# Kernel tuning notes

Hardware: AMD Instinct MI355X
Metric: run time of the kernel (lower is better)

Reference implementation:

```python
import jax, jax.numpy as jnp
import numpy as np

N_NODES = 100000
N_EDGES = 1600000
D = 128          # h_size == feature_representation_size
N_CLASSES = 2
N_GRAPHS = 64


def setup_inputs() -> dict:
    key = jax.random.key(0)
    ks = jax.random.split(key, 8)
    scale = 1.0 / np.sqrt(D)
    x = jax.random.normal(ks[0], (N_NODES, D), jnp.float32)
    edge_index = jax.random.randint(ks[1], (2, N_EDGES), 0, N_NODES, dtype=jnp.int64)
    batch = jnp.sort(jax.random.randint(ks[2], (N_NODES,), 0, N_GRAPHS, dtype=jnp.int64))
    W0 = jax.random.normal(ks[3], (D, D), jnp.float32) * scale
    W1 = jax.random.normal(ks[4], (D, D), jnp.float32) * scale
    W2 = jax.random.normal(ks[5], (D, D), jnp.float32) * scale
    Wf = jax.random.normal(ks[6], (D, N_CLASSES), jnp.float32) * scale
    return dict(
        x=x, edge_index=edge_index, batch=batch,
        W0=W0, b0=jnp.zeros((D,), jnp.float32),
        W1=W1, b1=jnp.zeros((D,), jnp.float32),
        W2=W2, b2=jnp.zeros((D,), jnp.float32),
        Wf=Wf, bf=jnp.zeros((N_CLASSES,), jnp.float32),
    )


def gcn_norm(edge_index, num_nodes):
    # add self loops, symmetric normalization D^{-1/2} A_hat D^{-1/2}
    src, dst = edge_index[0], edge_index[1]
    loop = jnp.arange(num_nodes, dtype=src.dtype)
    src = jnp.concatenate([src, loop])
    dst = jnp.concatenate([dst, loop])
    ew = jnp.ones(src.shape[0], jnp.float32)
    deg = jax.ops.segment_sum(ew, dst, num_segments=num_nodes)
    dinv = jnp.where(deg > 0, jax.lax.rsqrt(deg), 0.0)
    norm = dinv[src] * dinv[dst]  # [E+N]
    return src, dst, norm


def gcn_conv(h, W, b, src, dst, norm, num_nodes):
    h = h @ W                                   # linear transform
    msg = h[src] * norm[:, None]                # gather + scale over edges
    out = jax.ops.segment_sum(msg, dst, num_segments=num_nodes)  # scatter-add
    return out + b


def reference(x, edge_index, batch, W0, b0, W1, b1, W2, b2, Wf, bf):
    n = x.shape[0]
    src, dst, norm = gcn_norm(edge_index, n)
    h = jax.nn.relu(gcn_conv(x, W0, b0, src, dst, norm, n))
    h = jax.nn.relu(gcn_conv(h, W1, b1, src, dst, norm, n))
    h = gcn_conv(h, W2, b2, src, dst, norm, n)  # last layer, no relu
    pooled = jax.ops.segment_max(h, batch, num_segments=N_GRAPHS)  # global max pool
    return pooled @ Wf + bf
```

## Files before the change

kernel.cpp:

```cpp
#include <hip/hip_runtime.h>
#include <hip/hip_bf16.h>
#include <hip/hip_fp16.h>
#include <float.h>

#define D 128
#define NGRAPHS 64
#define BKSHIFT 9
#define BKNODES 512
#define MAXBK 256
#define PCH 4096

typedef _Float16 h8 __attribute__((ext_vector_type(8)));
typedef float f4 __attribute__((ext_vector_type(4)));

__device__ __forceinline__ unsigned fkey(float f){
  unsigned u = __float_as_uint(f);
  return (u & 0x80000000u) ? ~u : (u | 0x80000000u);
}
__device__ __forceinline__ float funkey(unsigned k){
  unsigned u = (k & 0x80000000u) ? (k ^ 0x80000000u) : ~k;
  return __uint_as_float(u);
}

__global__ __launch_bounds__(256) void k_bhist_w(const int* __restrict__ dst,
    int* __restrict__ bcnt, int E, int npart,
    const float* __restrict__ W0, const float* __restrict__ W1,
    const float* __restrict__ W2, _Float16* __restrict__ Wsw){
  if ((int)blockIdx.x >= npart){
    int layer = blockIdx.x - npart;
    const float* W = (layer == 0) ? W0 : (layer == 1) ? W1 : W2;
    _Float16* dstp = Wsw + (size_t)layer * 16384;
    int lane = threadIdx.x & 63;
    int quad = lane >> 4;
    int n    = lane & 15;
    for (int pair = (threadIdx.x >> 6); pair < 32; pair += 4){
      int k0 = pair >> 3;
      int tt = pair & 7;
      _Float16 v[8];
      #pragma unroll
      for (int j = 0; j < 8; j++){
        int k = k0 * 32 + quad * 8 + j;
        v[j] = (_Float16)W[k * 128 + 16 * tt + n];
      }
      *(uint4*)&dstp[((size_t)pair * 64 + lane) * 8] = *(uint4*)v;
    }
    return;
  }
  __shared__ int h[MAXBK];
  int t = threadIdx.x;
  for (int i = t; i < MAXBK; i += 256) h[i] = 0;
  __syncthreads();
  int e0 = blockIdx.x * PCH;
  #pragma unroll
  for (int j = 0; j < PCH / 256; j++){
    int e = e0 + t + j * 256;
    if (e < E) atomicAdd(&h[dst[e] >> BKSHIFT], 1);
  }
  __syncthreads();
  for (int i = t; i < MAXBK; i += 256) if (h[i]) atomicAdd(&bcnt[i], h[i]);
}

__global__ __launch_bounds__(256) void k_bscan(const int* __restrict__ bcnt,
    int* __restrict__ bOff, int* __restrict__ bCur, int* __restrict__ row_ptr,
    unsigned* __restrict__ pk, int nbk, int N, int E){
  __shared__ int sh[256];
  int t = threadIdx.x;
  for (int i = t; i < NGRAPHS * D; i += 256) pk[i] = 0u;
  int v = (t < nbk) ? bcnt[t] : 0;
  sh[t] = v; __syncthreads();
  for (int off = 1; off < 256; off <<= 1){
    int x = (t >= off) ? sh[t - off] : 0;
    __syncthreads();
    sh[t] += x;
    __syncthreads();
  }
  if (t < nbk){ int ex = sh[t] - v; bOff[t] = ex; bCur[t] = ex; }
  if (t == 0){ bOff[nbk] = E; row_ptr[N] = E; }
}

__global__ __launch_bounds__(256) void k_part(const int* __restrict__ src,
    const int* __restrict__ dst, int* __restrict__ bCur,
    uint2* __restrict__ epart, int E){
  __shared__ int scnt[MAXBK], soff[MAXBK], sbase[MAXBK], scur[MAXBK];
  __shared__ int stmp[256];
  __shared__ uint2 stage[PCH];
  int t = threadIdx.x;
  int e0 = blockIdx.x * PCH;
  int eN = E - e0; if (eN > PCH) eN = PCH;
  for (int i = t; i < MAXBK; i += 256){ scnt[i] = 0; scur[i] = 0; }
  __syncthreads();
  uint2 mye[PCH / 256];
  #pragma unroll
  for (int j = 0; j < PCH / 256; j++){
    int e = e0 + t + j * 256;
    if (e < E){
      mye[j].x = (unsigned)src[e];
      mye[j].y = (unsigned)dst[e];
      atomicAdd(&scnt[mye[j].y >> BKSHIFT], 1);
    }
  }
  __syncthreads();
  int v = scnt[t];
  stmp[t] = v; __syncthreads();
  for (int off = 1; off < 256; off <<= 1){
    int x = (t >= off) ? stmp[t - off] : 0;
    __syncthreads();
    stmp[t] += x;
    __syncthreads();
  }
  soff[t] = stmp[t] - v;
  if (v > 0) sbase[t] = atomicAdd(&bCur[t], v);
  __syncthreads();
  #pragma unroll
  for (int j = 0; j < PCH / 256; j++){
    int e = e0 + t + j * 256;
    if (e < E){
      int b = mye[j].y >> BKSHIFT;
      int l = atomicAdd(&scur[b], 1);
      stage[soff[b] + l] = mye[j];
    }
  }
  __syncthreads();
  for (int j = t; j < eN; j += 256){
    uint2 ed = stage[j];
    int b = (int)(ed.y >> BKSHIFT);
    epart[(size_t)sbase[b] + (j - soff[b])] = ed;
  }
}

__global__ __launch_bounds__(256) void k_bfill(const uint2* __restrict__ epart,
    const int* __restrict__ bOff, int* __restrict__ row_ptr,
    int* __restrict__ col, float* __restrict__ dinv, int N){
  __shared__ int hc[BKNODES], off[BKNODES], cur[BKNODES];
  __shared__ int stmp[256];
  int b = blockIdx.x, t = threadIdx.x;
  int base = bOff[b], cntE = bOff[b + 1] - base;
  int node0 = b << BKSHIFT;
  int nloc = N - node0; if (nloc > BKNODES) nloc = BKNODES;
  for (int i = t; i < BKNODES; i += 256) hc[i] = 0;
  __syncthreads();
  for (int j = t; j < cntE; j += 256){
    uint2 ed = epart[(size_t)base + j];
    atomicAdd(&hc[ed.y - node0], 1);
  }
  __syncthreads();
  int a0 = hc[2 * t], a1 = hc[2 * t + 1];
  int s = a0 + a1;
  stmp[t] = s; __syncthreads();
  for (int o = 1; o < 256; o <<= 1){
    int x = (t >= o) ? stmp[t - o] : 0;
    __syncthreads();
    stmp[t] += x;
    __syncthreads();
  }
  int ex = stmp[t] - s;
  off[2 * t] = ex; off[2 * t + 1] = ex + a0;
  __syncthreads();
  for (int i = t; i < nloc; i += 256){
    row_ptr[node0 + i] = base + off[i];
    dinv[node0 + i]    = rsqrtf((float)hc[i] + 1.0f);
    cur[i] = off[i];
  }
  __syncthreads();
  for (int j = t; j < cntE; j += 256){
    uint2 ed = epart[(size_t)base + j];
    int p = atomicAdd(&cur[ed.y - node0], 1);
    col[base + p] = (int)ed.x;
  }
}

__global__ __launch_bounds__(256) void gemm_mfma(const _Float16* __restrict__ A,
    const _Float16* __restrict__ Wsw, _Float16* __restrict__ C, int M){
  __shared__ _Float16 lds[4][16][136];
  int wave = threadIdx.x >> 6;
  int lane = threadIdx.x & 63;
  int quad = lane >> 4;
  int l15  = lane & 15;
  int m0 = blockIdx.x * 64 + wave * 16;
  if (m0 >= M) return;
  f4 acc[8] = {};
  h8 af[4];
  const _Float16* arow = A + (size_t)(m0 + l15) * D;
  #pragma unroll
  for (int k0 = 0; k0 < 4; k0++)
    af[k0] = *(const h8*)&arow[k0 * 32 + quad * 8];
  #pragma unroll
  for (int k0 = 0; k0 < 4; k0++){
    #pragma unroll
    for (int t = 0; t < 8; t++){
      h8 bf = *(const h8*)&Wsw[((size_t)(k0 * 8 + t) * 64 + lane) * 8];
      acc[t] = __builtin_amdgcn_mfma_f32_16x16x32_f16(af[k0], bf, acc[t], 0, 0, 0);
    }
  }
  #pragma unroll
  for (int t = 0; t < 8; t++){
    #pragma unroll
    for (int r = 0; r < 4; r++)
      lds[wave][quad * 4 + r][t * 16 + l15] = (_Float16)acc[t][r];
  }
  #pragma unroll
  for (int it = 0; it < 4; it++){
    int idx = it * 64 + lane;
    int row = idx >> 4;
    int ch  = idx & 15;
    *(uint4*)&C[(size_t)(m0 + row) * D + ch * 8] = *(uint4*)&lds[wave][row][ch * 8];
  }
}

__global__ __launch_bounds__(256) void gemm_mfma_f32A(const float* __restrict__ A,
    const _Float16* __restrict__ Wsw, _Float16* __restrict__ C, int M){
  __shared__ _Float16 lds[4][16][136];
  int wave = threadIdx.x >> 6;
  int lane = threadIdx.x & 63;
  int quad = lane >> 4;
  int l15  = lane & 15;
  int m0 = blockIdx.x * 64 + wave * 16;
  if (m0 >= M) return;
  f4 acc[8] = {};
  h8 af[4];
  const float* arow = A + (size_t)(m0 + l15) * D;
  #pragma unroll
  for (int k0 = 0; k0 < 4; k0++){
    float4 a = *(const float4*)&arow[k0 * 32 + quad * 8];
    float4 b = *(const float4*)&arow[k0 * 32 + quad * 8 + 4];
    __half2 p0 = __floats2half2_rn(a.x, a.y);
    __half2 p1 = __floats2half2_rn(a.z, a.w);
    __half2 p2 = __floats2half2_rn(b.x, b.y);
    __half2 p3 = __floats2half2_rn(b.z, b.w);
    union { uint4 u; h8 v; } cv;
    cv.u.x = *(unsigned*)&p0; cv.u.y = *(unsigned*)&p1;
    cv.u.z = *(unsigned*)&p2; cv.u.w = *(unsigned*)&p3;
    af[k0] = cv.v;
  }
  #pragma unroll
  for (int k0 = 0; k0 < 4; k0++){
    #pragma unroll
    for (int t = 0; t < 8; t++){
      h8 bf = *(const h8*)&Wsw[((size_t)(k0 * 8 + t) * 64 + lane) * 8];
      acc[t] = __builtin_amdgcn_mfma_f32_16x16x32_f16(af[k0], bf, acc[t], 0, 0, 0);
    }
  }
  #pragma unroll
  for (int t = 0; t < 8; t++){
    #pragma unroll
    for (int r = 0; r < 4; r++)
      lds[wave][quad * 4 + r][t * 16 + l15] = (_Float16)acc[t][r];
  }
  #pragma unroll
  for (int it = 0; it < 4; it++){
    int idx = it * 64 + lane;
    int row = idx >> 4;
    int ch  = idx & 15;
    *(uint4*)&C[(size_t)(m0 + row) * D + ch * 8] = *(uint4*)&lds[wave][row][ch * 8];
  }
}

__device__ __forceinline__ void accm(float* acc, uint4 u, float w){
  union { uint4 u; _Float16 h[8]; } cv;
  cv.u = u;
  #pragma unroll
  for (int k = 0; k < 8; k++)
    acc[k] += (float)cv.h[k] * w;
}

__global__ __launch_bounds__(256) void k_agg(const __half* __restrict__ t,
    const int* __restrict__ row_ptr, const int* __restrict__ col,
    const float* __restrict__ dinv, const float* __restrict__ bias,
    __half* __restrict__ outh, int relu, int N){
  int node = blockIdx.x * 4 + (threadIdx.x >> 6);
  if (node >= N) return;
  int lane = threadIdx.x & 63;
  int way  = lane >> 4;
  int cg   = (lane & 15) * 8;
  float di = dinv[node];
  int beg = row_ptr[node], end = row_ptr[node + 1];
  float acc[8] = {0.f,0.f,0.f,0.f,0.f,0.f,0.f,0.f};
  int j = beg + way;
  for (; j + 12 < end; j += 16){
    int s0 = col[j], s1 = col[j + 4], s2 = col[j + 8], s3 = col[j + 12];
    float w0 = dinv[s0] * di;
    float w1 = dinv[s1] * di;
    float w2 = dinv[s2] * di;
    float w3 = dinv[s3] * di;
    uint4 u0 = *(const uint4*)&t[(size_t)s0 * D + cg];
    uint4 u1 = *(const uint4*)&t[(size_t)s1 * D + cg];
    uint4 u2 = *(const uint4*)&t[(size_t)s2 * D + cg];
    uint4 u3 = *(const uint4*)&t[(size_t)s3 * D + cg];
    accm(acc, u0, w0);
    accm(acc, u1, w1);
    accm(acc, u2, w2);
    accm(acc, u3, w3);
  }
  for (; j < end; j += 4){
    int s = col[j];
    float w = dinv[s] * di;
    uint4 u = *(const uint4*)&t[(size_t)s * D + cg];
    accm(acc, u, w);
  }
  #pragma unroll
  for (int k = 0; k < 8; k++){
    acc[k] += __shfl_xor(acc[k], 16, 64);
    acc[k] += __shfl_xor(acc[k], 32, 64);
  }
  if (way == 0){
    uint4 su = *(const uint4*)&t[(size_t)node * D + cg];
    union { uint4 u; _Float16 h[8]; } sv; sv.u = su;
    float dii = di * di;
    float4 b0 = *(const float4*)&bias[cg];
    float4 b1 = *(const float4*)&bias[cg + 4];
    float bb[8] = {b0.x, b0.y, b0.z, b0.w, b1.x, b1.y, b1.z, b1.w};
    float o[8];
    #pragma unroll
    for (int k = 0; k < 8; k++)
      o[k] = acc[k] + (float)sv.h[k] * dii + bb[k];
    if (relu){
      #pragma unroll
      for (int k = 0; k < 8; k++) o[k] = fmaxf(o[k], 0.f);
    }
    __half2 p0 = __floats2half2_rn(o[0], o[1]);
    __half2 p1 = __floats2half2_rn(o[2], o[3]);
    __half2 p2 = __floats2half2_rn(o[4], o[5]);
    __half2 p3 = __floats2half2_rn(o[6], o[7]);
    uint4 u;
    u.x = *(unsigned*)&p0; u.y = *(unsigned*)&p1;
    u.z = *(unsigned*)&p2; u.w = *(unsigned*)&p3;
    *(uint4*)&outh[(size_t)node * D + cg] = u;
  }
}

__global__ __launch_bounds__(128) void k_pool(const __half* __restrict__ h,
    const int* __restrict__ batch, unsigned* __restrict__ pk, int N){
  int d = threadIdx.x;
  int n0 = blockIdx.x * 64;
  int nEnd = n0 + 64; if (nEnd > N) nEnd = N;
  float cur = -FLT_MAX;
  int curg = batch[n0];
  int n = n0;
  for (; n + 3 < nEnd; n += 4){
    const __half* r = &h[(size_t)n * D + d];
    __half v0 = r[0], v1 = r[D], v2 = r[2 * D], v3 = r[3 * D];
    int g0 = batch[n], g1 = batch[n + 1], g2 = batch[n + 2], g3 = batch[n + 3];
    if (g0 != curg){ atomicMax(&pk[curg * D + d], fkey(cur)); cur = -FLT_MAX; curg = g0; }
    cur = fmaxf(cur, __half2float(v0));
    if (g1 != curg){ atomicMax(&pk[curg * D + d], fkey(cur)); cur = -FLT_MAX; curg = g1; }
    cur = fmaxf(cur, __half2float(v1));
    if (g2 != curg){ atomicMax(&pk[curg * D + d], fkey(cur)); cur = -FLT_MAX; curg = g2; }
    cur = fmaxf(cur, __half2float(v2));
    if (g3 != curg){ atomicMax(&pk[curg * D + d], fkey(cur)); cur = -FLT_MAX; curg = g3; }
    cur = fmaxf(cur, __half2float(v3));
  }
  for (; n < nEnd; n++){
    int g = batch[n];
    if (g != curg){ atomicMax(&pk[curg * D + d], fkey(cur)); cur = -FLT_MAX; curg = g; }
    cur = fmaxf(cur, __half2float(h[(size_t)n * D + d]));
  }
  atomicMax(&pk[curg * D + d], fkey(cur));
}

__global__ __launch_bounds__(128) void k_final(const unsigned* __restrict__ pk,
    const float* __restrict__ Wf, const float* __restrict__ bf,
    float* __restrict__ out){
  int t = threadIdx.x;
  int g = t >> 1, c = t & 1;
  float s = bf[c];
  for (int k = 0; k < D; k++)
    s += funkey(pk[g * D + k]) * Wf[k * 2 + c];
  out[g * 2 + c] = s;
}

extern "C" void kernel_launch(void* const* d_in, const int* in_sizes, int n_in,
                              void* d_out, int out_size, void* d_ws, size_t ws_size,
                              hipStream_t stream){
  const float* x   = (const float*)d_in[0];
  const int*   ei  = (const int*)d_in[1];
  const int*   bat = (const int*)d_in[2];
  const float* W0  = (const float*)d_in[3];
  const float* b0  = (const float*)d_in[4];
  const float* W1  = (const float*)d_in[5];
  const float* b1  = (const float*)d_in[6];
  const float* W2  = (const float*)d_in[7];
  const float* b2  = (const float*)d_in[8];
  const float* Wf  = (const float*)d_in[9];
  const float* bf  = (const float*)d_in[10];
  int N = in_sizes[0] / D;
  int E = in_sizes[1] / 2;
  const int* srcp = ei;
  const int* dstp = ei + E;
  int nbk   = (N + BKNODES - 1) / BKNODES;
  int npart = (E + PCH - 1) / PCH;

  char* p = (char*)d_ws;
  auto alloc = [&](size_t bytes)->char*{
    char* r = p; p += (bytes + 255) & ~(size_t)255; return r;
  };
  float*     dinv    = (float*)alloc((size_t)N * 4);
  int*       row_ptr = (int*)alloc((size_t)(N + 1) * 4);
  int*       col     = (int*)alloc((size_t)E * 4);
  uint2*     epart   = (uint2*)alloc((size_t)E * 8);
  _Float16*  tmp     = (_Float16*)alloc((size_t)N * D * 2);
  _Float16*  h16     = (_Float16*)alloc((size_t)N * D * 2);
  _Float16*  Wsw     = (_Float16*)alloc((size_t)3 * 16384 * 2);
  unsigned*  pk      = (unsigned*)alloc((size_t)NGRAPHS * D * 4);
  int*       bcnt    = (int*)alloc((size_t)MAXBK * 4);
  int*       bOff    = (int*)alloc((size_t)(MAXBK + 1) * 4);
  int*       bCur    = (int*)alloc((size_t)MAXBK * 4);

  hipMemsetAsync(bcnt, 0, (size_t)MAXBK * 4, stream);

  k_bhist_w<<<npart + 3, 256, 0, stream>>>(dstp, bcnt, E, npart, W0, W1, W2, Wsw);
  k_bscan<<<1, 256, 0, stream>>>(bcnt, bOff, bCur, row_ptr, pk, nbk, N, E);
  k_part<<<npart, 256, 0, stream>>>(srcp, dstp, bCur, epart, E);
  k_bfill<<<nbk, 256, 0, stream>>>(epart, bOff, row_ptr, col, dinv, N);

  int gblocks = (N + 63) / 64;
  int ablocks = (N + 3) / 4;
  gemm_mfma_f32A<<<gblocks, 256, 0, stream>>>(x, Wsw, tmp, N);
  k_agg<<<ablocks, 256, 0, stream>>>((const __half*)tmp, row_ptr, col, dinv, b0, (__half*)h16, 1, N);
  gemm_mfma<<<gblocks, 256, 0, stream>>>(h16, Wsw + 16384, tmp, N);
  k_agg<<<ablocks, 256, 0, stream>>>((const __half*)tmp, row_ptr, col, dinv, b1, (__half*)h16, 1, N);
  gemm_mfma<<<gblocks, 256, 0, stream>>>(h16, Wsw + 32768, tmp, N);
  k_agg<<<ablocks, 256, 0, stream>>>((const __half*)tmp, row_ptr, col, dinv, b2, (__half*)h16, 0, N);
  k_pool<<<(N + 63) / 64, 128, 0, stream>>>((const __half*)h16, bat, pk, N);
  k_final<<<1, 128, 0, stream>>>(pk, Wf, bf, (float*)d_out);
}
```

Baseline: 412.5 us.

## Fuse aggregation with next-layer GEMM and merge first GEMM into histogram launch

Adds a kernel that aggregates 16 nodes per block, applies bias and ReLU, stages the rows in LDS, and multiplies them by the next layer's weights with MFMA. This removes the intermediate h16 round trip and two standalone GEMM launches. It also folds the layer-0 GEMM, the edge histogram and the W1/W2 conversion into one kernel, and moves the bcnt zeroing into a small W0 conversion kernel instead of a memset. The cost is that each aggregation block now handles 4 nodes per wave serially, which may reduce memory-level parallelism in the gather. A second ping-pong buffer is allocated.

```diff
diff --git a/kernel.cpp b/kernel.cpp
--- a/kernel.cpp
+++ b/kernel.cpp
@@ -22,42 +22,106 @@
   return __uint_as_float(u);
 }
 
-__global__ __launch_bounds__(256) void k_bhist_w(const int* __restrict__ dst,
-    int* __restrict__ bcnt, int E, int npart,
-    const float* __restrict__ W0, const float* __restrict__ W1,
-    const float* __restrict__ W2, _Float16* __restrict__ Wsw){
-  if ((int)blockIdx.x >= npart){
-    int layer = blockIdx.x - npart;
-    const float* W = (layer == 0) ? W0 : (layer == 1) ? W1 : W2;
-    _Float16* dstp = Wsw + (size_t)layer * 16384;
+__device__ __forceinline__ void wcvt_pair(const float* __restrict__ W,
+    _Float16* __restrict__ dstp, int pair, int lane){
+  int quad = lane >> 4;
+  int n    = lane & 15;
+  int k0 = pair >> 3;
+  int tt = pair & 7;
+  _Float16 v[8];
+  #pragma unroll
+  for (int j = 0; j < 8; j++){
+    int k = k0 * 32 + quad * 8 + j;
+    v[j] = (_Float16)W[k * 128 + 16 * tt + n];
+  }
+  *(uint4*)&dstp[((size_t)pair * 64 + lane) * 8] = *(uint4*)v;
+}
+
+__global__ __launch_bounds__(256) void k_wcvt0(const float* __restrict__ W0,
+    _Float16* __restrict__ Wsw, int* __restrict__ bcnt){
+  if (blockIdx.x == 0 && threadIdx.x < MAXBK) bcnt[threadIdx.x] = 0;
+  int lane = threadIdx.x & 63;
+  int pair = blockIdx.x * 4 + (threadIdx.x >> 6);
+  wcvt_pair(W0, Wsw, pair, lane);
+}
+
+__global__ __launch_bounds__(256) void k_mega(
+    const float* __restrict__ x, const _Float16* __restrict__ Wsw0,
+    _Float16* __restrict__ C, int M, int gb,
+    const int* __restrict__ dst, int* __restrict__ bcnt, int E, int npart,
+    const float* __restrict__ W1, const float* __restrict__ W2,
+    _Float16* __restrict__ Wsw12){
+  __shared__ __align__(16) char smraw[4 * 16 * 136 * 2];
+  int bid = blockIdx.x;
+  if (bid < gb){
+    _Float16 (*lds)[136] = (_Float16(*)[136])(smraw + (threadIdx.x >> 6) * 16 * 136 * 2);
     int lane = threadIdx.x & 63;
     int quad = lane >> 4;
-    int n    = lane & 15;
-    for (int pair = (threadIdx.x >> 6); pair < 32; pair += 4){
-      int k0 = pair >> 3;
-      int tt = pair & 7;
-      _Float16 v[8];
+    int l15  = lane & 15;
+    int m0 = bid * 64 + (threadIdx.x >> 6) * 16;
+    if (m0 >= M) return;
+    f4 acc[8] = {};
+    h8 af[4];
+    const float* arow = x + (size_t)(m0 + l15) * D;
+    #pragma unroll
+    for (int k0 = 0; k0 < 4; k0++){
+      float4 a = *(const float4*)&arow[k0 * 32 + quad * 8];
+      float4 b = *(const float4*)&arow[k0 * 32 + quad * 8 + 4];
+      __half2 p0 = __floats2half2_rn(a.x, a.y);
+      __half2 p1 = __floats2half2_rn(a.z, a.w);
+      __half2 p2 = __floats2half2_rn(b.x, b.y);
+      __half2 p3 = __floats2half2_rn(b.z, b.w);
+      union { uint4 u; h8 v; } cv;
+      cv.u.x = *(unsigned*)&p0; cv.u.y = *(unsigned*)&p1;
+      cv.u.z = *(unsigned*)&p2; cv.u.w = *(unsigned*)&p3;
+      af[k0] = cv.v;
+    }
+    #pragma unroll
+    for (int k0 = 0; k0 < 4; k0++){
       #pragma unroll
-      for (int j = 0; j < 8; j++){
-        int k = k0 * 32 + quad * 8 + j;
-        v[j] = (_Float16)W[k * 128 + 16 * tt + n];
+      for (int t = 0; t < 8; t++){
+        h8 bf = *(const h8*)&Wsw0[((size_t)(k0 * 8 + t) * 64 + lane) * 8];
+        acc[t] = __builtin_amdgcn_mfma_f32_16x16x32_f16(af[k0], bf, acc[t], 0, 0, 0);
       }
-      *(uint4*)&dstp[((size_t)pair * 64 + lane) * 8] = *(uint4*)v;
+    }
+    #pragma unroll
+    for (int t = 0; t < 8; t++){
+      #pragma unroll
+      for (int r = 0; r < 4; r++)
+        lds[quad * 4 + r][t * 16 + l15] = (_Float16)acc[t][r];
+    }
+    #pragma unroll
+    for (int it = 0; it < 4; it++){
+      int idx = it * 64 + lane;
+      int row = idx >> 4;
+      int ch  = idx & 15;
+      *(uint4*)&C[(size_t)(m0 + row) * D + ch * 8] = *(uint4*)&lds[row][ch * 8];
     }
     return;
   }
-  __shared__ int h[MAXBK];
-  int t = threadIdx.x;
-  for (int i = t; i < MAXBK; i += 256) h[i] = 0;
-  __syncthreads();
-  int e0 = blockIdx.x * PCH;
-  #pragma unroll
-  for (int j = 0; j < PCH / 256; j++){
-    int e = e0 + t + j * 256;
-    if (e < E) atomicAdd(&h[dst[e] >> BKSHIFT], 1);
-  }
-  __syncthreads();
-  for (int i = t; i < MAXBK; i += 256) if (h[i]) atomicAdd(&bcnt[i], h[i]);
+  bid -= gb;
+  if (bid < npart){
+    int* h = (int*)smraw;
+    int t = threadIdx.x;
+    for (int i = t; i < MAXBK; i += 256) h[i] = 0;
+    __syncthreads();
+    int e0 = bid * PCH;
+    #pragma unroll
+    for (int j = 0; j < PCH / 256; j++){
+      int e = e0 + t + j * 256;
+      if (e < E) atomicAdd(&h[dst[e] >> BKSHIFT], 1);
+    }
+    __syncthreads();
+    for (int i = t; i < MAXBK; i += 256) if (h[i]) atomicAdd(&bcnt[i], h[i]);
+    return;
+  }
+  bid -= npart;
+  const float* W = (bid < 2) ? W1 : W2;
+  _Float16* dstp = Wsw12 + ((bid < 2) ? 0 : 16384);
+  int pbase = (bid & 1) * 16;
+  int lane = threadIdx.x & 63;
+  for (int pp = (threadIdx.x >> 6); pp < 16; pp += 4)
+    wcvt_pair(W, dstp, pbase + pp, lane);
 }
 
 __global__ __launch_bounds__(256) void k_bscan(const int* __restrict__ bcnt,
@@ -169,92 +233,6 @@
   }
 }
 
-__global__ __launch_bounds__(256) void gemm_mfma(const _Float16* __restrict__ A,
-    const _Float16* __restrict__ Wsw, _Float16* __restrict__ C, int M){
-  __shared__ _Float16 lds[4][16][136];
-  int wave = threadIdx.x >> 6;
-  int lane = threadIdx.x & 63;
-  int quad = lane >> 4;
-  int l15  = lane & 15;
-  int m0 = blockIdx.x * 64 + wave * 16;
-  if (m0 >= M) return;
-  f4 acc[8] = {};
-  h8 af[4];
-  const _Float16* arow = A + (size_t)(m0 + l15) * D;
-  #pragma unroll
-  for (int k0 = 0; k0 < 4; k0++)
-    af[k0] = *(const h8*)&arow[k0 * 32 + quad * 8];
-  #pragma unroll
-  for (int k0 = 0; k0 < 4; k0++){
-    #pragma unroll
-    for (int t = 0; t < 8; t++){
-      h8 bf = *(const h8*)&Wsw[((size_t)(k0 * 8 + t) * 64 + lane) * 8];
-      acc[t] = __builtin_amdgcn_mfma_f32_16x16x32_f16(af[k0], bf, acc[t], 0, 0, 0);
-    }
-  }
-  #pragma unroll
-  for (int t = 0; t < 8; t++){
-    #pragma unroll
-    for (int r = 0; r < 4; r++)
-      lds[wave][quad * 4 + r][t * 16 + l15] = (_Float16)acc[t][r];
-  }
-  #pragma unroll
-  for (int it = 0; it < 4; it++){
-    int idx = it * 64 + lane;
-    int row = idx >> 4;
-    int ch  = idx & 15;
-    *(uint4*)&C[(size_t)(m0 + row) * D + ch * 8] = *(uint4*)&lds[wave][row][ch * 8];
-  }
-}
-
-__global__ __launch_bounds__(256) void gemm_mfma_f32A(const float* __restrict__ A,
-    const _Float16* __restrict__ Wsw, _Float16* __restrict__ C, int M){
-  __shared__ _Float16 lds[4][16][136];
-  int wave = threadIdx.x >> 6;
-  int lane = threadIdx.x & 63;
-  int quad = lane >> 4;
-  int l15  = lane & 15;
-  int m0 = blockIdx.x * 64 + wave * 16;
-  if (m0 >= M) return;
-  f4 acc[8] = {};
-  h8 af[4];
-  const float* arow = A + (size_t)(m0 + l15) * D;
-  #pragma unroll
-  for (int k0 = 0; k0 < 4; k0++){
-    float4 a = *(const float4*)&arow[k0 * 32 + quad * 8];
-    float4 b = *(const float4*)&arow[k0 * 32 + quad * 8 + 4];
-    __half2 p0 = __floats2half2_rn(a.x, a.y);
-    __half2 p1 = __floats2half2_rn(a.z, a.w);
-    __half2 p2 = __floats2half2_rn(b.x, b.y);
-    __half2 p3 = __floats2half2_rn(b.z, b.w);
-    union { uint4 u; h8 v; } cv;
-    cv.u.x = *(unsigned*)&p0; cv.u.y = *(unsigned*)&p1;
-    cv.u.z = *(unsigned*)&p2; cv.u.w = *(unsigned*)&p3;
-    af[k0] = cv.v;
-  }
-  #pragma unroll
-  for (int k0 = 0; k0 < 4; k0++){
-    #pragma unroll
-    for (int t = 0; t < 8; t++){
-      h8 bf = *(const h8*)&Wsw[((size_t)(k0 * 8 + t) * 64 + lane) * 8];
-      acc[t] = __builtin_amdgcn_mfma_f32_16x16x32_f16(af[k0], bf, acc[t], 0, 0, 0);
-    }
-  }
-  #pragma unroll
-  for (int t = 0; t < 8; t++){
-    #pragma unroll
-    for (int r = 0; r < 4; r++)
-      lds[wave][quad * 4 + r][t * 16 + l15] = (_Float16)acc[t][r];
-  }
-  #pragma unroll
-  for (int it = 0; it < 4; it++){
-    int idx = it * 64 + lane;
-    int row = idx >> 4;
-    int ch  = idx & 15;
-    *(uint4*)&C[(size_t)(m0 + row) * D + ch * 8] = *(uint4*)&lds[wave][row][ch * 8];
-  }
-}
-
 __device__ __forceinline__ void accm(float* acc, uint4 u, float w){
   union { uint4 u; _Float16 h[8]; } cv;
   cv.u = u;
@@ -263,18 +241,9 @@
     acc[k] += (float)cv.h[k] * w;
 }
 
-__global__ __launch_bounds__(256) void k_agg(const __half* __restrict__ t,
-    const int* __restrict__ row_ptr, const int* __restrict__ col,
-    const float* __restrict__ dinv, const float* __restrict__ bias,
-    __half* __restrict__ outh, int relu, int N){
-  int node = blockIdx.x * 4 + (threadIdx.x >> 6);
-  if (node >= N) return;
-  int lane = threadIdx.x & 63;
-  int way  = lane >> 4;
-  int cg   = (lane & 15) * 8;
-  float di = dinv[node];
-  int beg = row_ptr[node], end = row_ptr[node + 1];
-  float acc[8] = {0.f,0.f,0.f,0.f,0.f,0.f,0.f,0.f};
+__device__ __forceinline__ void agg_node(const __half* __restrict__ t,
+    const int* __restrict__ col, const float* __restrict__ dinv,
+    float di, int beg, int end, int way, int cg, float* acc){
   int j = beg + way;
   for (; j + 12 < end; j += 16){
     int s0 = col[j], s1 = col[j + 4], s2 = col[j + 8], s3 = col[j + 12];
@@ -297,6 +266,95 @@
     uint4 u = *(const uint4*)&t[(size_t)s * D + cg];
     accm(acc, u, w);
   }
+}
+
+__global__ __launch_bounds__(256) void k_agg_gemm(const __half* __restrict__ t,
+    const int* __restrict__ row_ptr, const int* __restrict__ col,
+    const float* __restrict__ dinv, const float* __restrict__ bias,
+    const _Float16* __restrict__ Wsw, _Float16* __restrict__ C, int N){
+  __shared__ _Float16 ldsA[16][136];
+  int tid = threadIdx.x;
+  int wave = tid >> 6;
+  int lane = tid & 63;
+  int way  = lane >> 4;
+  int l15  = lane & 15;
+  int cg   = l15 * 8;
+  int m0 = blockIdx.x * 16;
+  for (int nn = 0; nn < 4; nn++){
+    int node = m0 + wave * 4 + nn;
+    float acc[8] = {0.f,0.f,0.f,0.f,0.f,0.f,0.f,0.f};
+    float di = 0.f; int beg = 0, end = 0;
+    if (node < N){
+      di = dinv[node];
+      beg = row_ptr[node]; end = row_ptr[node + 1];
+    }
+    agg_node(t, col, dinv, di, beg, end, way, cg, acc);
+    #pragma unroll
+    for (int k = 0; k < 8; k++){
+      acc[k] += __shfl_xor(acc[k], 16, 64);
+      acc[k] += __shfl_xor(acc[k], 32, 64);
+    }
+    if (way == 0){
+      float o[8] = {0,0,0,0,0,0,0,0};
+      if (node < N){
+        uint4 su = *(const uint4*)&t[(size_t)node * D + cg];
+        union { uint4 u; _Float16 h[8]; } sv; sv.u = su;
+        float dii = di * di;
+        float4 b0 = *(const float4*)&bias[cg];
+        float4 b1 = *(const float4*)&bias[cg + 4];
+        float bb[8] = {b0.x, b0.y, b0.z, b0.w, b1.x, b1.y, b1.z, b1.w};
+        #pragma unroll
+        for (int k = 0; k < 8; k++)
+          o[k] = fmaxf(acc[k] + (float)sv.h[k] * dii + bb[k], 0.f);
+      }
+      __half2 p0 = __floats2half2_rn(o[0], o[1]);
+      __half2 p1 = __floats2half2_rn(o[2], o[3]);
+      __half2 p2 = __floats2half2_rn(o[4], o[5]);
+      __half2 p3 = __floats2half2_rn(o[6], o[7]);
+      uint4 u;
+      u.x = *(unsigned*)&p0; u.y = *(unsigned*)&p1;
+      u.z = *(unsigned*)&p2; u.w = *(unsigned*)&p3;
+      *(uint4*)&ldsA[wave * 4 + nn][cg] = u;
+    }
+  }
+  __syncthreads();
+  h8 af[4];
+  #pragma unroll
+  for (int k0 = 0; k0 < 4; k0++)
+    af[k0] = *(const h8*)&ldsA[l15][k0 * 32 + way * 8];
+  __syncthreads();
+  f4 a0 = {}, a1 = {};
+  #pragma unroll
+  for (int k0 = 0; k0 < 4; k0++){
+    h8 bf0 = *(const h8*)&Wsw[((size_t)(k0 * 8 + wave * 2    ) * 64 + lane) * 8];
+    h8 bf1 = *(const h8*)&Wsw[((size_t)(k0 * 8 + wave * 2 + 1) * 64 + lane) * 8];
+    a0 = __builtin_amdgcn_mfma_f32_16x16x32_f16(af[k0], bf0, a0, 0, 0, 0);
+    a1 = __builtin_amdgcn_mfma_f32_16x16x32_f16(af[k0], bf1, a1, 0, 0, 0);
+  }
+  #pragma unroll
+  for (int r = 0; r < 4; r++){
+    ldsA[way * 4 + r][(wave * 2    ) * 16 + l15] = (_Float16)a0[r];
+    ldsA[way * 4 + r][(wave * 2 + 1) * 16 + l15] = (_Float16)a1[r];
+  }
+  __syncthreads();
+  int row = tid >> 4, ch = tid & 15;
+  if (m0 + row < N)
+    *(uint4*)&C[(size_t)(m0 + row) * D + ch * 8] = *(uint4*)&ldsA[row][ch * 8];
+}
+
+__global__ __launch_bounds__(256) void k_agg(const __half* __restrict__ t,
+    const int* __restrict__ row_ptr, const int* __restrict__ col,
+    const float* __restrict__ dinv, const float* __restrict__ bias,
+    __half* __restrict__ outh, int N){
+  int node = blockIdx.x * 4 + (threadIdx.x >> 6);
+  if (node >= N) return;
+  int lane = threadIdx.x & 63;
+  int way  = lane >> 4;
+  int cg   = (lane & 15) * 8;
+  float di = dinv[node];
+  int beg = row_ptr[node], end = row_ptr[node + 1];
+  float acc[8] = {0.f,0.f,0.f,0.f,0.f,0.f,0.f,0.f};
+  agg_node(t, col, dinv, di, beg, end, way, cg, acc);
   #pragma unroll
   for (int k = 0; k < 8; k++){
     acc[k] += __shfl_xor(acc[k], 16, 64);
@@ -313,10 +371,6 @@
     #pragma unroll
     for (int k = 0; k < 8; k++)
       o[k] = acc[k] + (float)sv.h[k] * dii + bb[k];
-    if (relu){
-      #pragma unroll
-      for (int k = 0; k < 8; k++) o[k] = fmaxf(o[k], 0.f);
-    }
     __half2 p0 = __floats2half2_rn(o[0], o[1]);
     __half2 p1 = __floats2half2_rn(o[2], o[3]);
     __half2 p2 = __floats2half2_rn(o[4], o[5]);
@@ -388,6 +442,7 @@
   const int* dstp = ei + E;
   int nbk   = (N + BKNODES - 1) / BKNODES;
   int npart = (E + PCH - 1) / PCH;
+  int gb    = (N + 63) / 64;
 
   char* p = (char*)d_ws;
   auto alloc = [&](size_t bytes)->char*{
@@ -398,6 +453,7 @@
   int*       col     = (int*)alloc((size_t)E * 4);
   uint2*     epart   = (uint2*)alloc((size_t)E * 8);
   _Float16*  tmp     = (_Float16*)alloc((size_t)N * D * 2);
+  _Float16*  tmp2    = (_Float16*)alloc((size_t)N * D * 2);
   _Float16*  h16     = (_Float16*)alloc((size_t)N * D * 2);
   _Float16*  Wsw     = (_Float16*)alloc((size_t)3 * 16384 * 2);
   unsigned*  pk      = (unsigned*)alloc((size_t)NGRAPHS * D * 4);
@@ -405,21 +461,20 @@
   int*       bOff    = (int*)alloc((size_t)(MAXBK + 1) * 4);
   int*       bCur    = (int*)alloc((size_t)MAXBK * 4);
 
-  hipMemsetAsync(bcnt, 0, (size_t)MAXBK * 4, stream);
-
-  k_bhist_w<<<npart + 3, 256, 0, stream>>>(dstp, bcnt, E, npart, W0, W1, W2, Wsw);
+  k_wcvt0<<<8, 256, 0, stream>>>(W0, Wsw, bcnt);
+  k_mega<<<gb + npart + 4, 256, 0, stream>>>(x, Wsw, tmp, N, gb,
+      dstp, bcnt, E, npart, W1, W2, Wsw + 16384);
   k_bscan<<<1, 256, 0, stream>>>(bcnt, bOff, bCur, row_ptr, pk, nbk, N, E);
   k_part<<<npart, 256, 0, stream>>>(srcp, dstp, bCur, epart, E);
   k_bfill<<<nbk, 256, 0, stream>>>(epart, bOff, row_ptr, col, dinv, N);
 
-  int gblocks = (N + 63) / 64;
-  int ablocks = (N + 3) / 4;
-  gemm_mfma_f32A<<<gblocks, 256, 0, stream>>>(x, Wsw, tmp, N);
-  k_agg<<<ablocks, 256, 0, stream>>>((const __half*)tmp, row_ptr, col, dinv, b0, (__half*)h16, 1, N);
-  gemm_mfma<<<gblocks, 256, 0, stream>>>(h16, Wsw + 16384, tmp, N);
-  k_agg<<<ablocks, 256, 0, stream>>>((const __half*)tmp, row_ptr, col, dinv, b1, (__half*)h16, 1, N);
-  gemm_mfma<<<gblocks, 256, 0, stream>>>(h16, Wsw + 32768, tmp, N);
-  k_agg<<<ablocks, 256, 0, stream>>>((const __half*)tmp, row_ptr, col, dinv, b2, (__half*)h16, 0, N);
+  int fblocks = (N + 15) / 16;
+  k_agg_gemm<<<fblocks, 256, 0, stream>>>((const __half*)tmp, row_ptr, col,
+      dinv, b0, Wsw + 16384, tmp2, N);
+  k_agg_gemm<<<fblocks, 256, 0, stream>>>((const __half*)tmp2, row_ptr, col,
+      dinv, b1, Wsw + 32768, tmp, N);
+  k_agg<<<(N + 3) / 4, 256, 0, stream>>>((const __half*)tmp, row_ptr, col,
+      dinv, b2, (__half*)h16, N);
   k_pool<<<(N + 63) / 64, 128, 0, stream>>>((const __half*)h16, bat, pk, N);
   k_final<<<1, 128, 0, stream>>>(pk, Wf, bf, (float*)d_out);
 }
```

Result: no change. 409.0 us (-0.8%).

## Store features in channel-sliced layout and restructure aggregation for cache locality

Applied to the files above, without the earlier changes.

Node features are stored as eight 16-channel slices, each a contiguous N×16 array. The aggregation kernel now processes one slice per block, so the gathered working set per slice (N×32 bytes) can stay in L2/LLC across random neighbor reads. The first-layer GEMM is merged with the histogram and weight-conversion work into one launch, and the bcnt memset moves into a small W0-conversion kernel. The risks are more passes over the CSR structure (col, dinv and row_ptr are read eight times) and smaller 8-byte gathers.

```diff
diff --git a/kernel.cpp b/kernel.cpp
--- a/kernel.cpp
+++ b/kernel.cpp
@@ -13,6 +13,7 @@
 typedef _Float16 h8 __attribute__((ext_vector_type(8)));
 typedef float f4 __attribute__((ext_vector_type(4)));
 
+
 __device__ __forceinline__ unsigned fkey(float f){
   unsigned u = __float_as_uint(f);
   return (u & 0x80000000u) ? ~u : (u | 0x80000000u);
@@ -22,42 +23,113 @@
   return __uint_as_float(u);
 }
 
-__global__ __launch_bounds__(256) void k_bhist_w(const int* __restrict__ dst,
-    int* __restrict__ bcnt, int E, int npart,
-    const float* __restrict__ W0, const float* __restrict__ W1,
-    const float* __restrict__ W2, _Float16* __restrict__ Wsw){
-  if ((int)blockIdx.x >= npart){
-    int layer = blockIdx.x - npart;
-    const float* W = (layer == 0) ? W0 : (layer == 1) ? W1 : W2;
-    _Float16* dstp = Wsw + (size_t)layer * 16384;
+__device__ __forceinline__ void wcvt_pair(const float* __restrict__ W,
+    _Float16* __restrict__ dstp, int pair, int lane){
+  int quad = lane >> 4;
+  int n    = lane & 15;
+  int k0 = pair >> 3;
+  int tt = pair & 7;
+  _Float16 v[8];
+  #pragma unroll
+  for (int j = 0; j < 8; j++){
+    int k = k0 * 32 + quad * 8 + j;
+    v[j] = (_Float16)W[k * 128 + 16 * tt + n];
+  }
+  *(uint4*)&dstp[((size_t)pair * 64 + lane) * 8] = *(uint4*)v;
+}
+
+__global__ __launch_bounds__(256) void k_wcvt0(const float* __restrict__ W0,
+    _Float16* __restrict__ Wsw, int* __restrict__ bcnt){
+  if (blockIdx.x == 0 && threadIdx.x < MAXBK) bcnt[threadIdx.x] = 0;
+  int lane = threadIdx.x & 63;
+  int pair = blockIdx.x * 4 + (threadIdx.x >> 6);
+  wcvt_pair(W0, Wsw, pair, lane);
+}
+
+__device__ __forceinline__ void store_sliced(_Float16 (*lds)[136],
+    _Float16* __restrict__ CS, size_t sstr, int m0, int lane){
+  #pragma unroll
+  for (int it = 0; it < 4; it++){
+    int u = it * 64 + lane;
+    int slice = u & 7;
+    int half  = (u >> 3) & 1;
+    int row   = u >> 4;
+    *(uint4*)&CS[(size_t)slice * sstr + (size_t)(m0 + row) * 16 + half * 8] =
+        *(uint4*)&lds[row][slice * 16 + half * 8];
+  }
+}
+
+__global__ __launch_bounds__(256) void k_mega(
+    const float* __restrict__ x, const _Float16* __restrict__ Wsw0,
+    _Float16* __restrict__ CS, int M, int gb,
+    const int* __restrict__ dst, int* __restrict__ bcnt, int E, int npart,
+    const float* __restrict__ W1, const float* __restrict__ W2,
+    _Float16* __restrict__ Wsw12){
+  __shared__ __align__(16) char smraw[4 * 16 * 136 * 2];
+  int bid = blockIdx.x;
+  if (bid < gb){
+    _Float16 (*lds)[136] = (_Float16(*)[136])(smraw + (threadIdx.x >> 6) * 16 * 136 * 2);
     int lane = threadIdx.x & 63;
     int quad = lane >> 4;
-    int n    = lane & 15;
-    for (int pair = (threadIdx.x >> 6); pair < 32; pair += 4){
-      int k0 = pair >> 3;
-      int tt = pair & 7;
-      _Float16 v[8];
+    int l15  = lane & 15;
+    int m0 = bid * 64 + (threadIdx.x >> 6) * 16;
+    if (m0 >= M) return;
+    f4 acc[8] = {};
+    h8 af[4];
+    const float* arow = x + (size_t)(m0 + l15) * D;
+    #pragma unroll
+    for (int k0 = 0; k0 < 4; k0++){
+      float4 a = *(const float4*)&arow[k0 * 32 + quad * 8];
+      float4 b = *(const float4*)&arow[k0 * 32 + quad * 8 + 4];
+      __half2 p0 = __floats2half2_rn(a.x, a.y);
+      __half2 p1 = __floats2half2_rn(a.z, a.w);
+      __half2 p2 = __floats2half2_rn(b.x, b.y);
+      __half2 p3 = __floats2half2_rn(b.z, b.w);
+      union { uint4 u; h8 v; } cv;
+      cv.u.x = *(unsigned*)&p0; cv.u.y = *(unsigned*)&p1;
+      cv.u.z = *(unsigned*)&p2; cv.u.w = *(unsigned*)&p3;
+      af[k0] = cv.v;
+    }
+    #pragma unroll
+    for (int k0 = 0; k0 < 4; k0++){
       #pragma unroll
-      for (int j = 0; j < 8; j++){
-        int k = k0 * 32 + quad * 8 + j;
-        v[j] = (_Float16)W[k * 128 + 16 * tt + n];
+      for (int t = 0; t < 8; t++){
+        h8 bf = *(const h8*)&Wsw0[((size_t)(k0 * 8 + t) * 64 + lane) * 8];
+        acc[t] = __builtin_amdgcn_mfma_f32_16x16x32_f16(af[k0], bf, acc[t], 0, 0, 0);
       }
-      *(uint4*)&dstp[((size_t)pair * 64 + lane) * 8] = *(uint4*)v;
-    }
+    }
+    #pragma unroll
+    for (int t = 0; t < 8; t++){
+      #pragma unroll
+      for (int r = 0; r < 4; r++)
+        lds[quad * 4 + r][t * 16 + l15] = (_Float16)acc[t][r];
+    }
+    store_sliced(lds, CS, (size_t)M * 16, m0, lane);
     return;
   }
-  __shared__ int h[MAXBK];
-  int t = threadIdx.x;
-  for (int i = t; i < MAXBK; i += 256) h[i] = 0;
-  __syncthreads();
-  int e0 = blockIdx.x * PCH;
-  #pragma unroll
-  for (int j = 0; j < PCH / 256; j++){
-    int e = e0 + t + j * 256;
-    if (e < E) atomicAdd(&h[dst[e] >> BKSHIFT], 1);
-  }
-  __syncthreads();
-  for (int i = t; i < MAXBK; i += 256) if (h[i]) atomicAdd(&bcnt[i], h[i]);
+  bid -= gb;
+  if (bid < npart){
+    int* h = (int*)smraw;
+    int t = threadIdx.x;
+    for (int i = t; i < MAXBK; i += 256) h[i] = 0;
+    __syncthreads();
+    int e0 = bid * PCH;
+    #pragma unroll
+    for (int j = 0; j < PCH / 256; j++){
+      int e = e0 + t + j * 256;
+      if (e < E) atomicAdd(&h[dst[e] >> BKSHIFT], 1);
+    }
+    __syncthreads();
+    for (int i = t; i < MAXBK; i += 256) if (h[i]) atomicAdd(&bcnt[i], h[i]);
+    return;
+  }
+  bid -= npart;
+  const float* W = (bid < 2) ? W1 : W2;
+  _Float16* dstp = Wsw12 + ((bid < 2) ? 0 : 16384);
+  int pbase = (bid & 1) * 16;
+  int lane = threadIdx.x & 63;
+  for (int pp = (threadIdx.x >> 6); pp < 16; pp += 4)
+    wcvt_pair(W, dstp, pbase + pp, lane);
 }
 
 __global__ __launch_bounds__(256) void k_bscan(const int* __restrict__ bcnt,
@@ -169,8 +241,8 @@
   }
 }
 
-__global__ __launch_bounds__(256) void gemm_mfma(const _Float16* __restrict__ A,
-    const _Float16* __restrict__ Wsw, _Float16* __restrict__ C, int M){
+__global__ __launch_bounds__(256) void gemm_mfma(const _Float16* __restrict__ AS,
+    const _Float16* __restrict__ Wsw, _Float16* __restrict__ CS, int M){
   __shared__ _Float16 lds[4][16][136];
   int wave = threadIdx.x >> 6;
   int lane = threadIdx.x & 63;
@@ -178,12 +250,14 @@
   int l15  = lane & 15;
   int m0 = blockIdx.x * 64 + wave * 16;
   if (m0 >= M) return;
+  size_t sstr = (size_t)M * 16;
   f4 acc[8] = {};
   h8 af[4];
-  const _Float16* arow = A + (size_t)(m0 + l15) * D;
-  #pragma unroll
-  for (int k0 = 0; k0 < 4; k0++)
-    af[k0] = *(const h8*)&arow[k0 * 32 + quad * 8];
+  #pragma unroll
+  for (int k0 = 0; k0 < 4; k0++){
+    int sl = k0 * 2 + (quad >> 1);
+    af[k0] = *(const h8*)&AS[(size_t)sl * sstr + (size_t)(m0 + l15) * 16 + (quad & 1) * 8];
+  }
   #pragma unroll
   for (int k0 = 0; k0 < 4; k0++){
     #pragma unroll
@@ -198,161 +272,110 @@
     for (int r = 0; r < 4; r++)
       lds[wave][quad * 4 + r][t * 16 + l15] = (_Float16)acc[t][r];
   }
-  #pragma unroll
-  for (int it = 0; it < 4; it++){
-    int idx = it * 64 + lane;
-    int row = idx >> 4;
-    int ch  = idx & 15;
-    *(uint4*)&C[(size_t)(m0 + row) * D + ch * 8] = *(uint4*)&lds[wave][row][ch * 8];
-  }
-}
-
-__global__ __launch_bounds__(256) void gemm_mfma_f32A(const float* __restrict__ A,
-    const _Float16* __restrict__ Wsw, _Float16* __restrict__ C, int M){
-  __shared__ _Float16 lds[4][16][136];
-  int wave = threadIdx.x >> 6;
-  int lane = threadIdx.x & 63;
-  int quad = lane >> 4;
-  int l15  = lane & 15;
-  int m0 = blockIdx.x * 64 + wave * 16;
-  if (m0 >= M) return;
-  f4 acc[8] = {};
-  h8 af[4];
-  const float* arow = A + (size_t)(m0 + l15) * D;
-  #pragma unroll
-  for (int k0 = 0; k0 < 4; k0++){
-    float4 a = *(const float4*)&arow[k0 * 32 + quad * 8];
-    float4 b = *(const float4*)&arow[k0 * 32 + quad * 8 + 4];
-    __half2 p0 = __floats2half2_rn(a.x, a.y);
-    __half2 p1 = __floats2half2_rn(a.z, a.w);
-    __half2 p2 = __floats2half2_rn(b.x, b.y);
-    __half2 p3 = __floats2half2_rn(b.z, b.w);
-    union { uint4 u; h8 v; } cv;
-    cv.u.x = *(unsigned*)&p0; cv.u.y = *(unsigned*)&p1;
-    cv.u.z = *(unsigned*)&p2; cv.u.w = *(unsigned*)&p3;
-    af[k0] = cv.v;
-  }
-  #pragma unroll
-  for (int k0 = 0; k0 < 4; k0++){
-    #pragma unroll
-    for (int t = 0; t < 8; t++){
-      h8 bf = *(const h8*)&Wsw[((size_t)(k0 * 8 + t) * 64 + lane) * 8];
-      acc[t] = __builtin_amdgcn_mfma_f32_16x16x32_f16(af[k0], bf, acc[t], 0, 0, 0);
-    }
-  }
-  #pragma unroll
-  for (int t = 0; t < 8; t++){
-    #pragma unroll
-    for (int r = 0; r < 4; r++)
-      lds[wave][quad * 4 + r][t * 16 + l15] = (_Float16)acc[t][r];
-  }
-  #pragma unroll
-  for (int it = 0; it < 4; it++){
-    int idx = it * 64 + lane;
-    int row = idx >> 4;
-    int ch  = idx & 15;
-    *(uint4*)&C[(size_t)(m0 + row) * D + ch * 8] = *(uint4*)&lds[wave][row][ch * 8];
-  }
-}
-
-__device__ __forceinline__ void accm(float* acc, uint4 u, float w){
-  union { uint4 u; _Float16 h[8]; } cv;
+  store_sliced(lds[wave], CS, sstr, m0, lane);
+}
+
+__device__ __forceinline__ void acc4(float* a, uint2 u, float w){
+  union { uint2 u; _Float16 h[4]; } cv;
   cv.u = u;
   #pragma unroll
-  for (int k = 0; k < 8; k++)
-    acc[k] += (float)cv.h[k] * w;
-}
-
-__global__ __launch_bounds__(256) void k_agg(const __half* __restrict__ t,
+  for (int k = 0; k < 4; k++)
+    a[k] += (float)cv.h[k] * w;
+}
+
+__global__ __launch_bounds__(256) void k_aggS(const _Float16* __restrict__ tS,
     const int* __restrict__ row_ptr, const int* __restrict__ col,
     const float* __restrict__ dinv, const float* __restrict__ bias,
-    __half* __restrict__ outh, int relu, int N){
-  int node = blockIdx.x * 4 + (threadIdx.x >> 6);
-  if (node >= N) return;
-  int lane = threadIdx.x & 63;
-  int way  = lane >> 4;
-  int cg   = (lane & 15) * 8;
-  float di = dinv[node];
-  int beg = row_ptr[node], end = row_ptr[node + 1];
-  float acc[8] = {0.f,0.f,0.f,0.f,0.f,0.f,0.f,0.f};
-  int j = beg + way;
-  for (; j + 12 < end; j += 16){
-    int s0 = col[j], s1 = col[j + 4], s2 = col[j + 8], s3 = col[j + 12];
-    float w0 = dinv[s0] * di;
-    float w1 = dinv[s1] * di;
-    float w2 = dinv[s2] * di;
-    float w3 = dinv[s3] * di;
-    uint4 u0 = *(const uint4*)&t[(size_t)s0 * D + cg];
-    uint4 u1 = *(const uint4*)&t[(size_t)s1 * D + cg];
-    uint4 u2 = *(const uint4*)&t[(size_t)s2 * D + cg];
-    uint4 u3 = *(const uint4*)&t[(size_t)s3 * D + cg];
-    accm(acc, u0, w0);
-    accm(acc, u1, w1);
-    accm(acc, u2, w2);
-    accm(acc, u3, w3);
-  }
-  for (; j < end; j += 4){
-    int s = col[j];
-    float w = dinv[s] * di;
-    uint4 u = *(const uint4*)&t[(size_t)s * D + cg];
-    accm(acc, u, w);
-  }
-  #pragma unroll
-  for (int k = 0; k < 8; k++){
-    acc[k] += __shfl_xor(acc[k], 16, 64);
-    acc[k] += __shfl_xor(acc[k], 32, 64);
-  }
-  if (way == 0){
-    uint4 su = *(const uint4*)&t[(size_t)node * D + cg];
-    union { uint4 u; _Float16 h[8]; } sv; sv.u = su;
-    float dii = di * di;
-    float4 b0 = *(const float4*)&bias[cg];
-    float4 b1 = *(const float4*)&bias[cg + 4];
-    float bb[8] = {b0.x, b0.y, b0.z, b0.w, b1.x, b1.y, b1.z, b1.w};
-    float o[8];
-    #pragma unroll
-    for (int k = 0; k < 8; k++)
-      o[k] = acc[k] + (float)sv.h[k] * dii + bb[k];
-    if (relu){
+    _Float16* __restrict__ outS, int relu, int N){
+  int slice = blockIdx.x & 7;
+  int chunk = blockIdx.x >> 3;
+  int wavei = threadIdx.x >> 6;
+  int lane  = threadIdx.x & 63;
+  int way   = lane >> 2;
+  int cq    = (lane & 3) * 4;
+  size_t sstr = (size_t)N * 16;
+  const _Float16* ts = tS + (size_t)slice * sstr;
+  _Float16* os = outS + (size_t)slice * sstr;
+  float4 b4 = *(const float4*)&bias[slice * 16 + cq];
+  float bb[4] = {b4.x, b4.y, b4.z, b4.w};
+  int node0 = chunk * 32 + wavei * 8;
+  int nodeEnd = node0 + 8; if (nodeEnd > N) nodeEnd = N;
+  for (int node = node0; node < nodeEnd; node++){
+    float di = dinv[node];
+    int beg = row_ptr[node], end = row_ptr[node + 1];
+    float a[4] = {0.f, 0.f, 0.f, 0.f};
+    int j = beg + way;
+    for (; j + 16 < end; j += 32){
+      int s0 = col[j], s1 = col[j + 16];
+      float w0 = dinv[s0] * di;
+      float w1 = dinv[s1] * di;
+      uint2 u0 = *(const uint2*)&ts[(size_t)s0 * 16 + cq];
+      uint2 u1 = *(const uint2*)&ts[(size_t)s1 * 16 + cq];
+      acc4(a, u0, w0);
+      acc4(a, u1, w1);
+    }
+    if (j < end){
+      int s = col[j];
+      float w = dinv[s] * di;
+      uint2 u = *(const uint2*)&ts[(size_t)s * 16 + cq];
+      acc4(a, u, w);
+    }
+    #pragma unroll
+    for (int k = 0; k < 4; k++){
+      a[k] += __shfl_xor(a[k], 4, 64);
+      a[k] += __shfl_xor(a[k], 8, 64);
+      a[k] += __shfl_xor(a[k], 16, 64);
+      a[k] += __shfl_xor(a[k], 32, 64);
+    }
+    if (way == 0){
+      uint2 su = *(const uint2*)&ts[(size_t)node * 16 + cq];
+      union { uint2 u; _Float16 h[4]; } sv; sv.u = su;
+      float dii = di * di;
+      float o[4];
       #pragma unroll
-      for (int k = 0; k < 8; k++) o[k] = fmaxf(o[k], 0.f);
-    }
-    __half2 p0 = __floats2half2_rn(o[0], o[1]);
-    __half2 p1 = __floats2half2_rn(o[2], o[3]);
-    __half2 p2 = __floats2half2_rn(o[4], o[5]);
-    __half2 p3 = __floats2half2_rn(o[6], o[7]);
-    uint4 u;
-    u.x = *(unsigned*)&p0; u.y = *(unsigned*)&p1;
-    u.z = *(unsigned*)&p2; u.w = *(unsigned*)&p3;
-    *(uint4*)&outh[(size_t)node * D + cg] = u;
-  }
-}
-
-__global__ __launch_bounds__(128) void k_pool(const __half* __restrict__ h,
+      for (int k = 0; k < 4; k++)
+        o[k] = a[k] + (float)sv.h[k] * dii + bb[k];
+      if (relu){
+        #pragma unroll
+        for (int k = 0; k < 4; k++) o[k] = fmaxf(o[k], 0.f);
+      }
+      __half2 p0 = __floats2half2_rn(o[0], o[1]);
+      __half2 p1 = __floats2half2_rn(o[2], o[3]);
+      uint2 u;
+      u.x = *(unsigned*)&p0;
+      u.y = *(unsigned*)&p1;
+      *(uint2*)&os[(size_t)node * 16 + cq] = u;
+    }
+  }
+}
+
+__global__ __launch_bounds__(128) void k_pool(const _Float16* __restrict__ hS,
     const int* __restrict__ batch, unsigned* __restrict__ pk, int N){
   int d = threadIdx.x;
+  int slice = d >> 4, c = d & 15;
+  const _Float16* hs = hS + (size_t)slice * N * 16 + c;
   int n0 = blockIdx.x * 64;
   int nEnd = n0 + 64; if (nEnd > N) nEnd = N;
   float cur = -FLT_MAX;
   int curg = batch[n0];
   int n = n0;
   for (; n + 3 < nEnd; n += 4){
-    const __half* r = &h[(size_t)n * D + d];
-    __half v0 = r[0], v1 = r[D], v2 = r[2 * D], v3 = r[3 * D];
+    const _Float16* r = &hs[(size_t)n * 16];
+    _Float16 v0 = r[0], v1 = r[16], v2 = r[32], v3 = r[48];
     int g0 = batch[n], g1 = batch[n + 1], g2 = batch[n + 2], g3 = batch[n + 3];
     if (g0 != curg){ atomicMax(&pk[curg * D + d], fkey(cur)); cur = -FLT_MAX; curg = g0; }
-    cur = fmaxf(cur, __half2float(v0));
+    cur = fmaxf(cur, (float)v0);
     if (g1 != curg){ atomicMax(&pk[curg * D + d], fkey(cur)); cur = -FLT_MAX; curg = g1; }
-    cur = fmaxf(cur, __half2float(v1));
+    cur = fmaxf(cur, (float)v1);
     if (g2 != curg){ atomicMax(&pk[curg * D + d], fkey(cur)); cur = -FLT_MAX; curg = g2; }
-    cur = fmaxf(cur, __half2float(v2));
+    cur = fmaxf(cur, (float)v2);
     if (g3 != curg){ atomicMax(&pk[curg * D + d], fkey(cur)); cur = -FLT_MAX; curg = g3; }
-    cur = fmaxf(cur, __half2float(v3));
+    cur = fmaxf(cur, (float)v3);
   }
   for (; n < nEnd; n++){
     int g = batch[n];
     if (g != curg){ atomicMax(&pk[curg * D + d], fkey(cur)); cur = -FLT_MAX; curg = g; }
-    cur = fmaxf(cur, __half2float(h[(size_t)n * D + d]));
+    cur = fmaxf(cur, (float)hs[(size_t)n * 16]);
   }
   atomicMax(&pk[curg * D + d], fkey(cur));
 }
@@ -388,6 +411,7 @@
   const int* dstp = ei + E;
   int nbk   = (N + BKNODES - 1) / BKNODES;
   int npart = (E + PCH - 1) / PCH;
+  int gb    = (N + 63) / 64;
 
   char* p = (char*)d_ws;
   auto alloc = [&](size_t bytes)->char*{
@@ -397,29 +421,27 @@
   int*       row_ptr = (int*)alloc((size_t)(N + 1) * 4);
   int*       col     = (int*)alloc((size_t)E * 4);
   uint2*     epart   = (uint2*)alloc((size_t)E * 8);
-  _Float16*  tmp     = (_Float16*)alloc((size_t)N * D * 2);
-  _Float16*  h16     = (_Float16*)alloc((size_t)N * D * 2);
+  _Float16*  S1      = (_Float16*)alloc((size_t)N * D * 2);
+  _Float16*  S2      = (_Float16*)alloc((size_t)N * D * 2);
   _Float16*  Wsw     = (_Float16*)alloc((size_t)3 * 16384 * 2);
   unsigned*  pk      = (unsigned*)alloc((size_t)NGRAPHS * D * 4);
   int*       bcnt    = (int*)alloc((size_t)MAXBK * 4);
   int*       bOff    = (int*)alloc((size_t)(MAXBK + 1) * 4);
   int*       bCur    = (int*)alloc((size_t)MAXBK * 4);
 
-  hipMemsetAsync(bcnt, 0, (size_t)MAXBK * 4, stream);
-
-  k_bhist_w<<<npart + 3, 256, 0, stream>>>(dstp, bcnt, E, npart, W0, W1, W2, Wsw);
+  k_wcvt0<<<8, 256, 0, stream>>>(W0, Wsw, bcnt);
+  k_mega<<<gb + npart + 4, 256, 0, stream>>>(x, Wsw, S1, N, gb,
+      dstp, bcnt, E, npart, W1, W2, Wsw + 16384);
   k_bscan<<<1, 256, 0, stream>>>(bcnt, bOff, bCur, row_ptr, pk, nbk, N, E);
   k_part<<<npart, 256, 0, stream>>>(srcp, dstp, bCur, epart, E);
   k_bfill<<<nbk, 256, 0, stream>>>(epart, bOff, row_ptr, col, dinv, N);
 
-  int gblocks = (N + 63) / 64;
-  int ablocks = (N + 3) / 4;
-  gemm_mfma_f32A<<<gblocks, 256, 0, stream>>>(x, Wsw, tmp, N);
-  k_agg<<<ablocks, 256, 0, stream>>>((const __half*)tmp, row_ptr, col, dinv, b0, (__half*)h16, 1, N);
-  gemm_mfma<<<gblocks, 256, 0, stream>>>(h16, Wsw + 16384, tmp, N);
-  k_agg<<<ablocks, 256, 0, stream>>>((const __half*)tmp, row_ptr, col, dinv, b1, (__half*)h16, 1, N);
-  gemm_mfma<<<gblocks, 256, 0, stream>>>(h16, Wsw + 32768, tmp, N);
-  k_agg<<<ablocks, 256, 0, stream>>>((const __half*)tmp, row_ptr, col, dinv, b2, (__half*)h16, 0, N);
-  k_pool<<<(N + 63) / 64, 128, 0, stream>>>((const __half*)h16, bat, pk, N);
+  int ablocks = ((N + 31) / 32) * 8;
+  k_aggS<<<ablocks, 256, 0, stream>>>(S1, row_ptr, col, dinv, b0, S2, 1, N);
+  gemm_mfma<<<gb, 256, 0, stream>>>(S2, Wsw + 16384, S1, N);
+  k_aggS<<<ablocks, 256, 0, stream>>>(S1, row_ptr, col, dinv, b1, S2, 1, N);
+  gemm_mfma<<<gb, 256, 0, stream>>>(S2, Wsw + 32768, S1, N);
+  k_aggS<<<ablocks, 256, 0, stream>>>(S1, row_ptr, col, dinv, b2, S2, 0, N);
+  k_pool<<<(N + 63) / 64, 128, 0, stream>>>(S2, bat, pk, N);
   k_final<<<1, 128, 0, stream>>>(pk, Wf, bf, (float*)d_out);
 }
```

Measured after the change: 869.3 us. +110.7%, slower.
